# Kernel tuning notes

Hardware: AMD Instinct MI355X
Metric: run time of the kernel (lower is better)

The kernel has to match this reference:

```python
import jax, jax.numpy as jnp
import numpy as np

N_NODES = 50000
N_EDGES = 1600000
F_IN = 512      # 2 * embedding_dimension
HID = 512
OUT = 4
NEG_SLOPE = 0.01  # torch LeakyReLU default


def _leaky_relu(x):
    return jnp.where(x >= 0, x, NEG_SLOPE * x)


def setup_inputs() -> dict:
    key = jax.random.key(0)
    ks = jax.random.split(key, 12)
    s_in = 1.0 / np.sqrt(F_IN)
    s_h = 1.0 / np.sqrt(HID)
    return {
        "feature": jax.random.normal(ks[0], (N_NODES, F_IN), jnp.float32),
        "edge_index": jax.random.randint(ks[1], (2, N_EDGES), 0, N_NODES, jnp.int64),
        "edge_type": jax.random.randint(ks[2], (N_EDGES,), 0, 2, jnp.int64),
        # input MLP
        "W_in": jax.random.uniform(ks[3], (F_IN, HID), jnp.float32, -s_in, s_in),
        "b_in": jnp.zeros((HID,), jnp.float32),
        # sage1: lin_l (bias) on aggregated neighbors, lin_r (no bias) on self
        "W1_l": jax.random.uniform(ks[4], (HID, HID), jnp.float32, -s_h, s_h),
        "b1_l": jnp.zeros((HID,), jnp.float32),
        "W1_r": jax.random.uniform(ks[5], (HID, HID), jnp.float32, -s_h, s_h),
        # sage2
        "W2_l": jax.random.uniform(ks[6], (HID, HID), jnp.float32, -s_h, s_h),
        "b2_l": jnp.zeros((HID,), jnp.float32),
        "W2_r": jax.random.uniform(ks[7], (HID, HID), jnp.float32, -s_h, s_h),
        # output linear (hidden -> 4); note forward skips linear_relu_output1
        "W_out": jax.random.uniform(ks[8], (HID, OUT), jnp.float32, -s_h, s_h),
        "b_out": jnp.zeros((OUT,), jnp.float32),
    }


def _sage_conv(x, src, dst, W_l, b_l, W_r):
    # mean aggregation of source features onto destinations (PyG default flow)
    agg = jax.ops.segment_sum(x[src], dst, num_segments=N_NODES)  # [N, H]
    cnt = jax.ops.segment_sum(jnp.ones((src.shape[0], 1), x.dtype), dst,
                              num_segments=N_NODES)               # [N, 1]
    mean = agg / jnp.maximum(cnt, 1.0)
    return mean @ W_l + b_l + x @ W_r


def reference(feature, edge_index, edge_type,
              W_in, b_in, W1_l, b1_l, W1_r, W2_l, b2_l, W2_r, W_out, b_out):
    src, dst = edge_index[0], edge_index[1]
    x = _leaky_relu(feature.astype(jnp.float32) @ W_in + b_in)
    x = _sage_conv(x, src, dst, W1_l, b1_l, W1_r)
    # dropout is identity in eval mode
    x = _sage_conv(x, src, dst, W2_l, b2_l, W2_r)
    return x @ W_out + b_out
```

## Files before the change

kernel.cpp:

```cpp
#include <hip/hip_runtime.h>
#include <stdint.h>

#define NNODES 50000
#define NEDGES 1600000
#define HID 512
#define MPAD 50048
#define NEG_SLOPE 0.01f
#define NBUCK 98
#define NBLK 200
#define TILE 8000
#define NSUB 8

typedef __attribute__((ext_vector_type(8))) short bf16x8;
typedef __attribute__((ext_vector_type(8))) unsigned short u16x8;
typedef __attribute__((ext_vector_type(4))) float f32x4;

__device__ __forceinline__ float bf2f(unsigned short u) {
  unsigned int x = ((unsigned int)u) << 16;
  return __builtin_bit_cast(float, x);
}
__device__ __forceinline__ unsigned short f2bf(float f) {
  unsigned int u = __builtin_bit_cast(unsigned int, f);
  u += 0x7FFFu + ((u >> 16) & 1u);
  return (unsigned short)(u >> 16);
}
__device__ __forceinline__ void gload_lds16(const void* g, void* l) {
  __builtin_amdgcn_global_load_lds(
      (const __attribute__((address_space(1))) void*)g,
      (__attribute__((address_space(3))) void*)l, 16, 0, 0);
}

__global__ void flagk(const int* __restrict__ ei, int* __restrict__ flag) {
  int t = threadIdx.x;
  unsigned long long m = __ballot(ei[2 * t + 1] != 0);
  if (t == 0) *flag = (m != 0ULL) ? 1 : 0;
}

__global__ __launch_bounds__(256) void histk(const int* __restrict__ ei,
                                             const int* __restrict__ flag,
                                             int* __restrict__ hist) {
  __shared__ int h[NBUCK];
  int t = threadIdx.x, blk = blockIdx.x;
  for (int i = t; i < NBUCK; i += 256) h[i] = 0;
  __syncthreads();
  int f = *flag;
  int e0 = blk * TILE;
  for (int e = e0 + t; e < e0 + TILE; e += 256) {
    int d = f ? ei[(size_t)NEDGES + e] : ei[2 * ((size_t)NEDGES + e)];
    if ((unsigned)d < NNODES) atomicAdd(&h[d >> 9], 1);
  }
  __syncthreads();
  for (int i = t; i < NBUCK; i += 256) hist[i * NBLK + blk] = h[i];
}

__global__ __launch_bounds__(512) void scanh(int* __restrict__ hist,
                                             int* __restrict__ bstart) {
  __shared__ int s[512];
  const int TOT = NBUCK * NBLK;
  const int C = 40;
  int t = threadIdx.x;
  int base = t * C;
  int sum = 0;
#pragma unroll
  for (int i = 0; i < C; i++) {
    int idx = base + i;
    sum += (idx < TOT) ? hist[idx] : 0;
  }
  s[t] = sum;
  __syncthreads();
  for (int off = 1; off < 512; off <<= 1) {
    int u = (t >= off) ? s[t - off] : 0;
    __syncthreads();
    s[t] += u;
    __syncthreads();
  }
  int run = (t > 0) ? s[t - 1] : 0;
#pragma unroll
  for (int i = 0; i < C; i++) {
    int idx = base + i;
    if (idx < TOT) {
      int v = hist[idx];
      hist[idx] = run;
      if (idx % NBLK == 0) bstart[idx / NBLK] = run;
      run += v;
    }
  }
  if (t == 511) bstart[NBUCK] = s[511];
}

__global__ __launch_bounds__(256) void binscatter(const int* __restrict__ ei,
                                                  const int* __restrict__ flag,
                                                  const int* __restrict__ hbase,
                                                  unsigned int* __restrict__ pcol) {
  __shared__ int lb[NBUCK];
  int t = threadIdx.x, blk = blockIdx.x;
  for (int i = t; i < NBUCK; i += 256) lb[i] = hbase[i * NBLK + blk];
  __syncthreads();
  int f = *flag;
  int e0 = blk * TILE;
  for (int e = e0 + t; e < e0 + TILE; e += 256) {
    int sN = f ? ei[e] : ei[2 * (size_t)e];
    int d  = f ? ei[(size_t)NEDGES + e] : ei[2 * ((size_t)NEDGES + e)];
    if ((unsigned)d >= NNODES) continue;
    if ((unsigned)sN >= NNODES) sN = 0;
    int pos = atomicAdd(&lb[d >> 9], 1);
    pcol[pos] = ((unsigned)(d & 511) << 16) | (unsigned)sN;
  }
}

__global__ void tcast(const float* __restrict__ w, unsigned short* __restrict__ wt) {
  int i = blockIdx.x * 256 + threadIdx.x;
  int n = i >> 9, k = i & 511;
  wt[i] = f2bf(w[(k << 9) | n]);
}

__device__ __forceinline__ float wave_dot(const float* __restrict__ Arow,
                                          const float* __restrict__ B, int j) {
  int l = threadIdx.x & 63;
  float4 a0 = *reinterpret_cast<const float4*>(Arow + l * 8);
  float4 a1 = *reinterpret_cast<const float4*>(Arow + l * 8 + 4);
  const float* bb = B + (size_t)(l * 8) * 4 + j;
  float s = a0.x * bb[0] + a0.y * bb[4] + a0.z * bb[8] + a0.w * bb[12] +
            a1.x * bb[16] + a1.y * bb[20] + a1.z * bb[24] + a1.w * bb[28];
#pragma unroll
  for (int off = 1; off < 64; off <<= 1) s += __shfl_xor(s, off);
  return s;
}

__global__ __launch_bounds__(256) void smallA(
    const float* __restrict__ W2l, const float* __restrict__ W2r,
    const float* __restrict__ Wout, const float* __restrict__ b2l,
    const float* __restrict__ bout,
    float* __restrict__ Wlp, float* __restrict__ Wrp, float* __restrict__ bp) {
  int gw = blockIdx.x * 4 + (threadIdx.x >> 6);
  int l = threadIdx.x & 63;
  if (gw < 2048) {
    float v = wave_dot(W2l + (size_t)(gw >> 2) * 512, Wout, gw & 3);
    if (l == 0) Wlp[gw] = v;
  } else if (gw < 4096) {
    int g = gw - 2048;
    float v = wave_dot(W2r + (size_t)(g >> 2) * 512, Wout, g & 3);
    if (l == 0) Wrp[g] = v;
  } else if (gw < 4100) {
    int j = gw - 4096;
    float v = wave_dot(b2l, Wout, j);
    if (l == 0) bp[j] = v + bout[j];
  }
}

__global__ __launch_bounds__(256) void smallB(
    const float* __restrict__ W1l, const float* __restrict__ W1r,
    const float* __restrict__ b1l,
    const float* __restrict__ Wlp, const float* __restrict__ Wrp,
    const float* __restrict__ bp,
    float* __restrict__ Pall, float* __restrict__ kb, float* __restrict__ kc) {
  int gw = blockIdx.x * 4 + (threadIdx.x >> 6);
  int l = threadIdx.x & 63;
  if (gw < 6144) {
    int k = gw / 12, jg = gw % 12;
    int g = jg >> 2, j = jg & 3;
    float v;
    if (g == 0) v = wave_dot(W1l + (size_t)k * 512, Wlp, j);
    else if (g == 1) v = wave_dot(W1r + (size_t)k * 512, Wlp, j) +
                         wave_dot(W1l + (size_t)k * 512, Wrp, j);
    else v = wave_dot(W1r + (size_t)k * 512, Wrp, j);
    if (l == 0) Pall[k * 12 + jg] = v;
  } else if (gw < 6152) {
    int i = gw - 6144, j = i & 3;
    if (i < 4) {
      float v = wave_dot(b1l, Wlp, j);
      if (l == 0) kb[j] = v;
    } else {
      float v = wave_dot(b1l, Wrp, j);
      if (l == 0) kc[j] = v + bp[j];
    }
  }
}

__global__ __launch_bounds__(256) void gemm1(
    const float* __restrict__ A, const unsigned short* __restrict__ Bt,
    const float* __restrict__ bias, unsigned short* __restrict__ C) {
  __shared__ unsigned short As[128 * 32];
  __shared__ unsigned short Bs[128 * 32];
  const int tid = threadIdx.x;
  const int wave = tid >> 6, lane = tid & 63;
  const int bid = blockIdx.x;
  const int bm = (bid >> 2) * 128, bn = (bid & 3) * 128;
  const int wr = wave >> 1, wc = wave & 1;
  const int r15 = lane & 15, kl = lane >> 4;
  const int srow = lane >> 2, soff = (lane & 3) * 8;

  f32x4 acc[4][4];
#pragma unroll
  for (int i = 0; i < 4; i++)
#pragma unroll
    for (int j = 0; j < 4; j++) acc[i][j] = {0.f, 0.f, 0.f, 0.f};

  for (int kt = 0; kt < HID / 32; ++kt) {
#pragma unroll
    for (int rr = 0; rr < 2; ++rr) {
      int c = wave * 2 + rr;
      int row = c * 16 + srow;
      gload_lds16(Bt + (size_t)(bn + row) * HID + kt * 32 + soff, (void*)&Bs[c * 512]);
    }
#pragma unroll
    for (int ss = 0; ss < 2; ++ss) {
      int s = tid + ss * 256;
      int row = s >> 2, k8 = (s & 3) * 8;
      int garow = bm + row;
      if (garow >= NNODES) garow = 0;
      const float* ga = A + (size_t)garow * HID + kt * 32 + k8;
      float4 v0 = *reinterpret_cast<const float4*>(ga);
      float4 v1 = *reinterpret_cast<const float4*>(ga + 4);
      u16x8 pk;
      pk[0] = f2bf(v0.x); pk[1] = f2bf(v0.y); pk[2] = f2bf(v0.z); pk[3] = f2bf(v0.w);
      pk[4] = f2bf(v1.x); pk[5] = f2bf(v1.y); pk[6] = f2bf(v1.z); pk[7] = f2bf(v1.w);
      *reinterpret_cast<u16x8*>(&As[row * 32 + k8]) = pk;
    }
    __syncthreads();
    bf16x8 af[4], bfr[4];
#pragma unroll
    for (int mi = 0; mi < 4; ++mi)
      af[mi] = *reinterpret_cast<const bf16x8*>(&As[(wr * 64 + mi * 16 + r15) * 32 + kl * 8]);
#pragma unroll
    for (int ni = 0; ni < 4; ++ni)
      bfr[ni] = *reinterpret_cast<const bf16x8*>(&Bs[(wc * 64 + ni * 16 + r15) * 32 + kl * 8]);
#pragma unroll
    for (int mi = 0; mi < 4; ++mi)
#pragma unroll
      for (int ni = 0; ni < 4; ++ni)
        acc[mi][ni] = __builtin_amdgcn_mfma_f32_16x16x32_bf16(af[mi], bfr[ni], acc[mi][ni], 0, 0, 0);
    __syncthreads();
  }
#pragma unroll
  for (int ni = 0; ni < 4; ++ni) {
    int col = bn + wc * 64 + ni * 16 + r15;
    float bv = bias[col];
#pragma unroll
    for (int mi = 0; mi < 4; ++mi) {
#pragma unroll
      for (int rg = 0; rg < 4; ++rg) {
        int row = bm + wr * 64 + mi * 16 + kl * 4 + rg;
        float v = acc[mi][ni][rg] + bv;
        v = (v >= 0.f) ? v : NEG_SLOPE * v;
        if (row < NNODES) C[(size_t)row * HID + col] = f2bf(v);
      }
    }
  }
}

__global__ __launch_bounds__(256) void proj12(
    const unsigned short* __restrict__ x0h, const float* __restrict__ Pall,
    float* __restrict__ t0) {
  const int lane = threadIdx.x & 63;
  const int wid = blockIdx.x * 4 + (threadIdx.x >> 6);
  const int nw = gridDim.x * 4;
  float4 P[24];
#pragma unroll
  for (int i = 0; i < 8; i++)
#pragma unroll
    for (int c = 0; c < 3; c++)
      P[i * 3 + c] = *reinterpret_cast<const float4*>(Pall + (size_t)(lane * 8 + i) * 12 + c * 4);

  for (int n = wid; n < NNODES; n += nw) {
    uint4 r = *reinterpret_cast<const uint4*>(x0h + (size_t)n * HID + lane * 8);
    float xv[8];
    unsigned int w[4] = {r.x, r.y, r.z, r.w};
#pragma unroll
    for (int d = 0; d < 4; d++) {
      xv[2 * d]     = __builtin_bit_cast(float, w[d] << 16);
      xv[2 * d + 1] = __builtin_bit_cast(float, w[d] & 0xFFFF0000u);
    }
    float acc[12];
#pragma unroll
    for (int j = 0; j < 12; j++) acc[j] = 0.f;
#pragma unroll
    for (int i = 0; i < 8; i++) {
#pragma unroll
      for (int c = 0; c < 3; c++) {
        acc[c * 4 + 0] += xv[i] * P[i * 3 + c].x;
        acc[c * 4 + 1] += xv[i] * P[i * 3 + c].y;
        acc[c * 4 + 2] += xv[i] * P[i * 3 + c].z;
        acc[c * 4 + 3] += xv[i] * P[i * 3 + c].w;
      }
    }
#pragma unroll
    for (int off = 1; off < 64; off <<= 1)
#pragma unroll
      for (int j = 0; j < 12; j++) acc[j] += __shfl_xor(acc[j], off);
    if (lane == 0) {
      float* o = t0 + (size_t)n * 12;
      *reinterpret_cast<float4*>(o)     = {acc[0], acc[1], acc[2], acc[3]};
      *reinterpret_cast<float4*>(o + 4) = {acc[4], acc[5], acc[6], acc[7]};
      *reinterpret_cast<float4*>(o + 8) = {acc[8], acc[9], acc[10], acc[11]};
    }
  }
}

__global__ __launch_bounds__(256) void aggA(
    const unsigned int* __restrict__ pcol, const int* __restrict__ bstart,
    const float* __restrict__ t0, float* __restrict__ partial) {
  __shared__ float tab[512 * 5];
  int t = threadIdx.x;
  int b = blockIdx.x >> 3, sb = blockIdx.x & 7;
  for (int i = t; i < 2560; i += 256) tab[i] = 0.f;
  __syncthreads();
  int st = bstart[b], en = bstart[b + 1];
  int len = en - st;
  int a0 = st + (int)(((long long)len * sb) >> 3);
  int a1 = st + (int)(((long long)len * (sb + 1)) >> 3);
  for (int e = a0 + t; e < a1; e += 256) {
    unsigned v = pcol[e];
    int i = v >> 16, src = v & 0xFFFF;
    float4 x = *reinterpret_cast<const float4*>(t0 + (size_t)src * 12);
    atomicAdd(&tab[i * 5 + 0], x.x);
    atomicAdd(&tab[i * 5 + 1], x.y);
    atomicAdd(&tab[i * 5 + 2], x.z);
    atomicAdd(&tab[i * 5 + 3], x.w);
    atomicAdd(&tab[i * 5 + 4], 1.f);
  }
  __syncthreads();
  float* o = partial + (size_t)blockIdx.x * 2560;
  for (int i = t; i < 2560; i += 256) o[i] = tab[i];
}

__global__ __launch_bounds__(256) void finA(
    const float* __restrict__ partial, const float* __restrict__ t0,
    float* __restrict__ s1, float* __restrict__ degf) {
  int n = blockIdx.x * 256 + threadIdx.x;
  if (n >= NNODES) return;
  int b = n >> 9, i = n & 511;
  float a[5] = {0.f, 0.f, 0.f, 0.f, 0.f};
#pragma unroll
  for (int s = 0; s < 8; s++) {
    const float* p = partial + (size_t)(b * 8 + s) * 2560 + i * 5;
#pragma unroll
    for (int j = 0; j < 5; j++) a[j] += p[j];
  }
  float deg = a[4];
  float sc = (deg > 0.f) ? 1.f / deg : 0.f;
  float4 tb = *reinterpret_cast<const float4*>(t0 + (size_t)n * 12 + 4);
  float4 o = {a[0] * sc + tb.x, a[1] * sc + tb.y, a[2] * sc + tb.z, a[3] * sc + tb.w};
  *reinterpret_cast<float4*>(s1 + (size_t)n * 4) = o;
  degf[n] = deg;
}

__global__ __launch_bounds__(256) void aggB(
    const unsigned int* __restrict__ pcol, const int* __restrict__ bstart,
    const float* __restrict__ s1, float* __restrict__ partial) {
  __shared__ float tab[512 * 4];
  int t = threadIdx.x;
  int b = blockIdx.x >> 3, sb = blockIdx.x & 7;
  for (int i = t; i < 2048; i += 256) tab[i] = 0.f;
  __syncthreads();
  int st = bstart[b], en = bstart[b + 1];
  int len = en - st;
  int a0 = st + (int)(((long long)len * sb) >> 3);
  int a1 = st + (int)(((long long)len * (sb + 1)) >> 3);
  for (int e = a0 + t; e < a1; e += 256) {
    unsigned v = pcol[e];
    int i = v >> 16, src = v & 0xFFFF;
    float4 x = *reinterpret_cast<const float4*>(s1 + (size_t)src * 4);
    atomicAdd(&tab[i * 4 + 0], x.x);
    atomicAdd(&tab[i * 4 + 1], x.y);
    atomicAdd(&tab[i * 4 + 2], x.z);
    atomicAdd(&tab[i * 4 + 3], x.w);
  }
  __syncthreads();
  float* o = partial + (size_t)blockIdx.x * 2048;
  for (int i = t; i < 2048; i += 256) o[i] = tab[i];
}

__global__ __launch_bounds__(256) void finB(
    const float* __restrict__ partial, const float* __restrict__ t0,
    const float* __restrict__ degf, const float* __restrict__ kb,
    const float* __restrict__ kc, float* __restrict__ out) {
  int n = blockIdx.x * 256 + threadIdx.x;
  if (n >= NNODES) return;
  int b = n >> 9, i = n & 511;
  float a[4] = {0.f, 0.f, 0.f, 0.f};
#pragma unroll
  for (int s = 0; s < 8; s++) {
    const float* p = partial + (size_t)(b * 8 + s) * 2048 + i * 4;
#pragma unroll
    for (int j = 0; j < 4; j++) a[j] += p[j];
  }
  float deg = degf[n];
  float sc = (deg > 0.f) ? 1.f / deg : 0.f;
  float ind = (deg > 0.f) ? 1.f : 0.f;
  float4 c = *reinterpret_cast<const float4*>(t0 + (size_t)n * 12 + 8);
  float4 vb = *reinterpret_cast<const float4*>(kb);
  float4 vc = *reinterpret_cast<const float4*>(kc);
  float4 o = {a[0] * sc + c.x + ind * vb.x + vc.x,
              a[1] * sc + c.y + ind * vb.y + vc.y,
              a[2] * sc + c.z + ind * vb.z + vc.z,
              a[3] * sc + c.w + ind * vb.w + vc.w};
  *reinterpret_cast<float4*>(out + (size_t)n * 4) = o;
}

extern "C" void kernel_launch(void* const* d_in, const int* in_sizes, int n_in,
                              void* d_out, int out_size, void* d_ws, size_t ws_size,
                              hipStream_t stream) {
  const float* feat = (const float*)d_in[0];
  const int* ei = (const int*)d_in[1];
  const float* W_in = (const float*)d_in[3];
  const float* b_in = (const float*)d_in[4];
  const float* W1l = (const float*)d_in[5];
  const float* b1l = (const float*)d_in[6];
  const float* W1r = (const float*)d_in[7];
  const float* W2l = (const float*)d_in[8];
  const float* b2l = (const float*)d_in[9];
  const float* W2r = (const float*)d_in[10];
  const float* Wout = (const float*)d_in[11];
  const float* bout = (const float*)d_in[12];
  float* out = (float*)d_out;

  char* ws = (char*)d_ws;
  size_t off = 0;
  auto alloc = [&](size_t bytes) {
    void* p = ws + off;
    off += (bytes + 15) & ~(size_t)15;
    return p;
  };
  int* flag   = (int*)alloc(16);
  int* hist   = (int*)alloc((size_t)NBUCK * NBLK * 4);
  int* bstart = (int*)alloc((NBUCK + 1) * 4);
  unsigned int* pcol = (unsigned int*)alloc((size_t)NEDGES * 4);
  unsigned short* Wt0 = (unsigned short*)alloc(512 * 512 * 2);
  float* Wlp  = (float*)alloc(2048 * 4);
  float* Wrp  = (float*)alloc(2048 * 4);
  float* bp   = (float*)alloc(16);
  float* Pall = (float*)alloc(512 * 12 * 4);
  float* kb   = (float*)alloc(16);
  float* kc   = (float*)alloc(16);
  float* t0   = (float*)alloc((size_t)NNODES * 12 * 4);
  float* s1   = (float*)alloc((size_t)NNODES * 4 * 4);
  float* degf = (float*)alloc((size_t)NNODES * 4);
  float* partial = (float*)alloc((size_t)NBUCK * NSUB * 2560 * 4);
  unsigned short* x0h = (unsigned short*)alloc((size_t)MPAD * HID * 2);
  (void)ws_size;

  flagk<<<1, 64, 0, stream>>>(ei, flag);
  histk<<<NBLK, 256, 0, stream>>>(ei, flag, hist);
  scanh<<<1, 512, 0, stream>>>(hist, bstart);
  binscatter<<<NBLK, 256, 0, stream>>>(ei, flag, hist, pcol);

  tcast<<<1024, 256, 0, stream>>>(W_in, Wt0);
  smallA<<<1025, 256, 0, stream>>>(W2l, W2r, Wout, b2l, bout, Wlp, Wrp, bp);
  smallB<<<1538, 256, 0, stream>>>(W1l, W1r, b1l, Wlp, Wrp, bp, Pall, kb, kc);

  gemm1<<<(MPAD / 128) * 4, 256, 0, stream>>>(feat, Wt0, b_in, x0h);
  proj12<<<1024, 256, 0, stream>>>(x0h, Pall, t0);
  aggA<<<NBUCK * NSUB, 256, 0, stream>>>(pcol, bstart, t0, partial);
  finA<<<(NNODES + 255) / 256, 256, 0, stream>>>(partial, t0, s1, degf);
  aggB<<<NBUCK * NSUB, 256, 0, stream>>>(pcol, bstart, s1, partial);
  finB<<<(NNODES + 255) / 256, 256, 0, stream>>>(partial, t0, degf, kb, kc, out);
}
```

Measured before the change: 349.2 us.

## Fuse input GEMM with 12-column projection to avoid materialising hidden activations

Merges gemm1 and proj12 into one kernel. Each 512-thread block computes a full 128x512 tile of the input layer, applies bias and LeakyReLU in registers, multiplies by the 512x12 projection Pall, and reduces the partials through shuffles and LDS atomics. The 50k x 512 bf16 intermediate is therefore never written to or re-read from global memory. It also pads the LDS row stride to 40 to reduce bank conflicts, and widens the edge-index loads in histk and binscatter to handle two edges per thread. In exchange, only 391 blocks with large accumulators run, so occupancy may be lower, and the B tile is now loaded with plain loads instead of direct-to-LDS loads.

```diff
diff --git a/kernel.cpp b/kernel.cpp
--- a/kernel.cpp
+++ b/kernel.cpp
@@ -4,12 +4,12 @@
 #define NNODES 50000
 #define NEDGES 1600000
 #define HID 512
-#define MPAD 50048
 #define NEG_SLOPE 0.01f
 #define NBUCK 98
 #define NBLK 200
 #define TILE 8000
 #define NSUB 8
+#define GPBLK 391
 
 typedef __attribute__((ext_vector_type(8))) short bf16x8;
 typedef __attribute__((ext_vector_type(8))) unsigned short u16x8;
@@ -23,11 +23,6 @@
   unsigned int u = __builtin_bit_cast(unsigned int, f);
   u += 0x7FFFu + ((u >> 16) & 1u);
   return (unsigned short)(u >> 16);
-}
-__device__ __forceinline__ void gload_lds16(const void* g, void* l) {
-  __builtin_amdgcn_global_load_lds(
-      (const __attribute__((address_space(1))) void*)g,
-      (__attribute__((address_space(3))) void*)l, 16, 0, 0);
 }
 
 __global__ void flagk(const int* __restrict__ ei, int* __restrict__ flag) {
@@ -45,9 +40,17 @@
   __syncthreads();
   int f = *flag;
   int e0 = blk * TILE;
-  for (int e = e0 + t; e < e0 + TILE; e += 256) {
-    int d = f ? ei[(size_t)NEDGES + e] : ei[2 * ((size_t)NEDGES + e)];
-    if ((unsigned)d < NNODES) atomicAdd(&h[d >> 9], 1);
+  for (int e = e0 + 2 * t; e < e0 + TILE; e += 512) {
+    int d0, d1;
+    if (f) {
+      int2 v = *reinterpret_cast<const int2*>(&ei[(size_t)NEDGES + e]);
+      d0 = v.x; d1 = v.y;
+    } else {
+      int4 v = *reinterpret_cast<const int4*>(&ei[2 * ((size_t)NEDGES + e)]);
+      d0 = v.x; d1 = v.z;
+    }
+    if ((unsigned)d0 < NNODES) atomicAdd(&h[d0 >> 9], 1);
+    if ((unsigned)d1 < NNODES) atomicAdd(&h[d1 >> 9], 1);
   }
   __syncthreads();
   for (int i = t; i < NBUCK; i += 256) hist[i * NBLK + blk] = h[i];
@@ -98,13 +101,27 @@
   __syncthreads();
   int f = *flag;
   int e0 = blk * TILE;
-  for (int e = e0 + t; e < e0 + TILE; e += 256) {
-    int sN = f ? ei[e] : ei[2 * (size_t)e];
-    int d  = f ? ei[(size_t)NEDGES + e] : ei[2 * ((size_t)NEDGES + e)];
-    if ((unsigned)d >= NNODES) continue;
-    if ((unsigned)sN >= NNODES) sN = 0;
-    int pos = atomicAdd(&lb[d >> 9], 1);
-    pcol[pos] = ((unsigned)(d & 511) << 16) | (unsigned)sN;
+  for (int e = e0 + 2 * t; e < e0 + TILE; e += 512) {
+    int s0, s1, d0, d1;
+    if (f) {
+      int2 vs = *reinterpret_cast<const int2*>(&ei[e]);
+      int2 vd = *reinterpret_cast<const int2*>(&ei[(size_t)NEDGES + e]);
+      s0 = vs.x; s1 = vs.y; d0 = vd.x; d1 = vd.y;
+    } else {
+      int4 vs = *reinterpret_cast<const int4*>(&ei[2 * (size_t)e]);
+      int4 vd = *reinterpret_cast<const int4*>(&ei[2 * ((size_t)NEDGES + e)]);
+      s0 = vs.x; s1 = vs.z; d0 = vd.x; d1 = vd.z;
+    }
+    if ((unsigned)d0 < NNODES) {
+      if ((unsigned)s0 >= NNODES) s0 = 0;
+      int pos = atomicAdd(&lb[d0 >> 9], 1);
+      pcol[pos] = ((unsigned)(d0 & 511) << 16) | (unsigned)s0;
+    }
+    if ((unsigned)d1 < NNODES) {
+      if ((unsigned)s1 >= NNODES) s1 = 0;
+      int pos = atomicAdd(&lb[d1 >> 9], 1);
+      pcol[pos] = ((unsigned)(d1 & 511) << 16) | (unsigned)s1;
+    }
   }
 }
 
@@ -177,123 +194,115 @@
   }
 }
 
-__global__ __launch_bounds__(256) void gemm1(
+__global__ __launch_bounds__(512) void gemmproj(
     const float* __restrict__ A, const unsigned short* __restrict__ Bt,
-    const float* __restrict__ bias, unsigned short* __restrict__ C) {
-  __shared__ unsigned short As[128 * 32];
-  __shared__ unsigned short Bs[128 * 32];
+    const float* __restrict__ bias, const float* __restrict__ Pall,
+    float* __restrict__ t0) {
+  __shared__ __align__(16) char smem[51200];
+  unsigned short* As = (unsigned short*)smem;
+  unsigned short* Bs = (unsigned short*)(smem + 10240);
+  __shared__ float tab[128 * 12];
   const int tid = threadIdx.x;
-  const int wave = tid >> 6, lane = tid & 63;
-  const int bid = blockIdx.x;
-  const int bm = (bid >> 2) * 128, bn = (bid & 3) * 128;
-  const int wr = wave >> 1, wc = wave & 1;
+  const int wv = tid >> 6, lane = tid & 63;
+  const int bm = blockIdx.x * 128;
+  const int wr = wv >> 2, wc = wv & 3;
   const int r15 = lane & 15, kl = lane >> 4;
-  const int srow = lane >> 2, soff = (lane & 3) * 8;
-
-  f32x4 acc[4][4];
-#pragma unroll
-  for (int i = 0; i < 4; i++)
-#pragma unroll
-    for (int j = 0; j < 4; j++) acc[i][j] = {0.f, 0.f, 0.f, 0.f};
-
-  for (int kt = 0; kt < HID / 32; ++kt) {
-#pragma unroll
-    for (int rr = 0; rr < 2; ++rr) {
-      int c = wave * 2 + rr;
-      int row = c * 16 + srow;
-      gload_lds16(Bt + (size_t)(bn + row) * HID + kt * 32 + soff, (void*)&Bs[c * 512]);
-    }
-#pragma unroll
-    for (int ss = 0; ss < 2; ++ss) {
-      int s = tid + ss * 256;
-      int row = s >> 2, k8 = (s & 3) * 8;
-      int garow = bm + row;
-      if (garow >= NNODES) garow = 0;
-      const float* ga = A + (size_t)garow * HID + kt * 32 + k8;
-      float4 v0 = *reinterpret_cast<const float4*>(ga);
-      float4 v1 = *reinterpret_cast<const float4*>(ga + 4);
-      u16x8 pk;
-      pk[0] = f2bf(v0.x); pk[1] = f2bf(v0.y); pk[2] = f2bf(v0.z); pk[3] = f2bf(v0.w);
-      pk[4] = f2bf(v1.x); pk[5] = f2bf(v1.y); pk[6] = f2bf(v1.z); pk[7] = f2bf(v1.w);
-      *reinterpret_cast<u16x8*>(&As[row * 32 + k8]) = pk;
+
+  for (int i = tid; i < 1536; i += 512) tab[i] = 0.f;
+
+  f32x4 acc[8][4];
+#pragma unroll
+  for (int ni = 0; ni < 8; ni++)
+#pragma unroll
+    for (int mi = 0; mi < 4; mi++) acc[ni][mi] = {0.f, 0.f, 0.f, 0.f};
+
+  const int arow = tid >> 2;
+  const int ak8 = (tid & 3) * 8;
+  int garow = bm + arow;
+  if (garow >= NNODES) garow = 0;
+  const float* gabase = A + (size_t)garow * HID + ak8;
+
+  for (int kt = 0; kt < 16; ++kt) {
+    const float* ga = gabase + kt * 32;
+    float4 v0 = *reinterpret_cast<const float4*>(ga);
+    float4 v1 = *reinterpret_cast<const float4*>(ga + 4);
+    u16x8 pk;
+    pk[0] = f2bf(v0.x); pk[1] = f2bf(v0.y); pk[2] = f2bf(v0.z); pk[3] = f2bf(v0.w);
+    pk[4] = f2bf(v1.x); pk[5] = f2bf(v1.y); pk[6] = f2bf(v1.z); pk[7] = f2bf(v1.w);
+    *reinterpret_cast<u16x8*>(&As[arow * 40 + ak8]) = pk;
+#pragma unroll
+    for (int i = 0; i < 4; ++i) {
+      int c = i * 512 + tid;
+      int n = c >> 2, slot = c & 3;
+      uint4 bv = *reinterpret_cast<const uint4*>(Bt + (size_t)n * HID + kt * 32 + slot * 8);
+      *reinterpret_cast<uint4*>(&Bs[n * 40 + slot * 8]) = bv;
     }
     __syncthreads();
-    bf16x8 af[4], bfr[4];
+    bf16x8 af[4], bfr[8];
 #pragma unroll
     for (int mi = 0; mi < 4; ++mi)
-      af[mi] = *reinterpret_cast<const bf16x8*>(&As[(wr * 64 + mi * 16 + r15) * 32 + kl * 8]);
-#pragma unroll
-    for (int ni = 0; ni < 4; ++ni)
-      bfr[ni] = *reinterpret_cast<const bf16x8*>(&Bs[(wc * 64 + ni * 16 + r15) * 32 + kl * 8]);
-#pragma unroll
-    for (int mi = 0; mi < 4; ++mi)
-#pragma unroll
-      for (int ni = 0; ni < 4; ++ni)
-        acc[mi][ni] = __builtin_amdgcn_mfma_f32_16x16x32_bf16(af[mi], bfr[ni], acc[mi][ni], 0, 0, 0);
+      af[mi] = *reinterpret_cast<const bf16x8*>(&As[(wr * 64 + mi * 16 + r15) * 40 + kl * 8]);
+#pragma unroll
+    for (int ni = 0; ni < 8; ++ni)
+      bfr[ni] = *reinterpret_cast<const bf16x8*>(&Bs[(wc * 128 + ni * 16 + r15) * 40 + kl * 8]);
+#pragma unroll
+    for (int ni = 0; ni < 8; ++ni)
+#pragma unroll
+      for (int mi = 0; mi < 4; ++mi)
+        acc[ni][mi] = __builtin_amdgcn_mfma_f32_16x16x32_bf16(bfr[ni], af[mi], acc[ni][mi], 0, 0, 0);
     __syncthreads();
   }
-#pragma unroll
-  for (int ni = 0; ni < 4; ++ni) {
-    int col = bn + wc * 64 + ni * 16 + r15;
-    float bv = bias[col];
+
+  float part[4][12];
+#pragma unroll
+  for (int mi = 0; mi < 4; ++mi)
+#pragma unroll
+    for (int j = 0; j < 12; ++j) part[mi][j] = 0.f;
+
+#pragma unroll
+  for (int ni = 0; ni < 8; ++ni) {
+    int nb = wc * 128 + ni * 16 + kl * 4;
+    float4 bv4 = *reinterpret_cast<const float4*>(bias + nb);
+    float bb[4] = {bv4.x, bv4.y, bv4.z, bv4.w};
+#pragma unroll
+    for (int rg = 0; rg < 4; ++rg) {
+      const float* Pc = Pall + (size_t)(nb + rg) * 12;
+      float4 p0 = *reinterpret_cast<const float4*>(Pc);
+      float4 p1 = *reinterpret_cast<const float4*>(Pc + 4);
+      float4 p2 = *reinterpret_cast<const float4*>(Pc + 8);
+#pragma unroll
+      for (int mi = 0; mi < 4; ++mi) {
+        float v = acc[ni][mi][rg] + bb[rg];
+        v = (v >= 0.f) ? v : NEG_SLOPE * v;
+        part[mi][0] += v * p0.x; part[mi][1] += v * p0.y;
+        part[mi][2] += v * p0.z; part[mi][3] += v * p0.w;
+        part[mi][4] += v * p1.x; part[mi][5] += v * p1.y;
+        part[mi][6] += v * p1.z; part[mi][7] += v * p1.w;
+        part[mi][8] += v * p2.x; part[mi][9] += v * p2.y;
+        part[mi][10] += v * p2.z; part[mi][11] += v * p2.w;
+      }
+    }
+  }
+#pragma unroll
+  for (int mi = 0; mi < 4; ++mi)
+#pragma unroll
+    for (int j = 0; j < 12; ++j) {
+      part[mi][j] += __shfl_xor(part[mi][j], 16);
+      part[mi][j] += __shfl_xor(part[mi][j], 32);
+    }
+  if (kl == 0) {
 #pragma unroll
     for (int mi = 0; mi < 4; ++mi) {
-#pragma unroll
-      for (int rg = 0; rg < 4; ++rg) {
-        int row = bm + wr * 64 + mi * 16 + kl * 4 + rg;
-        float v = acc[mi][ni][rg] + bv;
-        v = (v >= 0.f) ? v : NEG_SLOPE * v;
-        if (row < NNODES) C[(size_t)row * HID + col] = f2bf(v);
-      }
-    }
-  }
-}
-
-__global__ __launch_bounds__(256) void proj12(
-    const unsigned short* __restrict__ x0h, const float* __restrict__ Pall,
-    float* __restrict__ t0) {
-  const int lane = threadIdx.x & 63;
-  const int wid = blockIdx.x * 4 + (threadIdx.x >> 6);
-  const int nw = gridDim.x * 4;
-  float4 P[24];
-#pragma unroll
-  for (int i = 0; i < 8; i++)
-#pragma unroll
-    for (int c = 0; c < 3; c++)
-      P[i * 3 + c] = *reinterpret_cast<const float4*>(Pall + (size_t)(lane * 8 + i) * 12 + c * 4);
-
-  for (int n = wid; n < NNODES; n += nw) {
-    uint4 r = *reinterpret_cast<const uint4*>(x0h + (size_t)n * HID + lane * 8);
-    float xv[8];
-    unsigned int w[4] = {r.x, r.y, r.z, r.w};
-#pragma unroll
-    for (int d = 0; d < 4; d++) {
-      xv[2 * d]     = __builtin_bit_cast(float, w[d] << 16);
-      xv[2 * d + 1] = __builtin_bit_cast(float, w[d] & 0xFFFF0000u);
-    }
-    float acc[12];
-#pragma unroll
-    for (int j = 0; j < 12; j++) acc[j] = 0.f;
-#pragma unroll
-    for (int i = 0; i < 8; i++) {
-#pragma unroll
-      for (int c = 0; c < 3; c++) {
-        acc[c * 4 + 0] += xv[i] * P[i * 3 + c].x;
-        acc[c * 4 + 1] += xv[i] * P[i * 3 + c].y;
-        acc[c * 4 + 2] += xv[i] * P[i * 3 + c].z;
-        acc[c * 4 + 3] += xv[i] * P[i * 3 + c].w;
-      }
-    }
-#pragma unroll
-    for (int off = 1; off < 64; off <<= 1)
-#pragma unroll
-      for (int j = 0; j < 12; j++) acc[j] += __shfl_xor(acc[j], off);
-    if (lane == 0) {
-      float* o = t0 + (size_t)n * 12;
-      *reinterpret_cast<float4*>(o)     = {acc[0], acc[1], acc[2], acc[3]};
-      *reinterpret_cast<float4*>(o + 4) = {acc[4], acc[5], acc[6], acc[7]};
-      *reinterpret_cast<float4*>(o + 8) = {acc[8], acc[9], acc[10], acc[11]};
-    }
+      int r = wr * 64 + mi * 16 + r15;
+#pragma unroll
+      for (int j = 0; j < 12; ++j) atomicAdd(&tab[r * 12 + j], part[mi][j]);
+    }
+  }
+  __syncthreads();
+  for (int i = tid; i < 1536; i += 512) {
+    int r = i / 12;
+    int gr = bm + r;
+    if (gr < NNODES) t0[(size_t)gr * 12 + (i - r * 12)] = tab[i];
   }
 }
 
@@ -437,7 +446,6 @@
   float* s1   = (float*)alloc((size_t)NNODES * 4 * 4);
   float* degf = (float*)alloc((size_t)NNODES * 4);
   float* partial = (float*)alloc((size_t)NBUCK * NSUB * 2560 * 4);
-  unsigned short* x0h = (unsigned short*)alloc((size_t)MPAD * HID * 2);
   (void)ws_size;
 
   flagk<<<1, 64, 0, stream>>>(ei, flag);
@@ -449,8 +457,7 @@
   smallA<<<1025, 256, 0, stream>>>(W2l, W2r, Wout, b2l, bout, Wlp, Wrp, bp);
   smallB<<<1538, 256, 0, stream>>>(W1l, W1r, b1l, Wlp, Wrp, bp, Pall, kb, kc);
 
-  gemm1<<<(MPAD / 128) * 4, 256, 0, stream>>>(feat, Wt0, b_in, x0h);
-  proj12<<<1024, 256, 0, stream>>>(x0h, Pall, t0);
+  gemmproj<<<GPBLK, 512, 0, stream>>>(feat, Wt0, b_in, Pall, t0);
   aggA<<<NBUCK * NSUB, 256, 0, stream>>>(pcol, bstart, t0, partial);
   finA<<<(NNODES + 255) / 256, 256, 0, stream>>>(partial, t0, s1, degf);
   aggB<<<NBUCK * NSUB, 256, 0, stream>>>(pcol, bstart, s1, partial);
```

Result: faster. 284.5 us (-18.5%).
